# Performance work log

Hardware: AMD Instinct MI355X
Metric: run time of the kernel (lower is better)

The kernel has to match this reference:

```python
import jax, jax.numpy as jnp
import numpy as np

N, D, E = 100000, 128, 800000

def setup_inputs() -> dict:
    key = jax.random.key(0)
    k1, k2, k3, k4 = jax.random.split(key, 4)
    z = jax.random.normal(k1, (N, D), dtype=jnp.float32)
    edge_index = jax.random.randint(k2, (2, E), 0, N, dtype=jnp.int64)
    # PyTorch-style init scale for Linear layers (kaiming-uniform-ish via normal is fine for a numeric reference)
    W1 = jax.random.normal(k3, (2 * D, D), dtype=jnp.float32) * (1.0 / np.sqrt(2 * D))
    b1 = jnp.zeros((D,), dtype=jnp.float32)
    W2 = jax.random.normal(k4, (D, 1), dtype=jnp.float32) * (1.0 / np.sqrt(D))
    b2 = jnp.zeros((1,), dtype=jnp.float32)
    return {"z": z, "edge_index": edge_index, "W1": W1, "b1": b1, "W2": W2, "b2": b2}

def reference(z, edge_index, W1, b1, W2, b2):
    # row/col gather of node embeddings
    row, col = edge_index[0], edge_index[1]
    # cat([z[row], z[col]]) @ W1 == z[row] @ W1[:D] + z[col] @ W1[D:]
    # -> avoids materializing the [E, 2D] concatenated tensor
    d = z.shape[1]
    h = z[row] @ W1[:d] + z[col] @ W1[d:] + b1          # [E, D]
    h = jax.nn.relu(h)                                   # Dropout(0.1) is identity in eval mode
    out = h @ W2 + b2                                    # [E, 1]
    return out.squeeze(-1)                               # [E]
```

## Files before the change

### kernel.cpp

```cpp
#include <hip/hip_runtime.h>

#define DDIM 128

typedef __bf16 bf16x8 __attribute__((ext_vector_type(8)));
typedef float  floatx4 __attribute__((ext_vector_type(4)));

__device__ inline unsigned short f2bf(float f) {
    unsigned u = __builtin_bit_cast(unsigned, f);
    u += 0x7fffu + ((u >> 16) & 1u);
    return (unsigned short)(u >> 16);
}

#define EPI_B 136

__global__ __launch_bounds__(256) void precompute_uv_mfma_q8(
    const float* __restrict__ z, const float* __restrict__ W1,
    const float* __restrict__ b1,
    signed char* __restrict__ U8, signed char* __restrict__ V8,
    float* __restrict__ u_scale, float* __restrict__ v_scale,
    int N, int nchunks)
{
    __shared__ unsigned short WsF[32 * 64 * 8];
    __shared__ __attribute__((aligned(16))) unsigned char epi[64 * EPI_B];

    const int t    = threadIdx.x;
    const int lane = t & 63;
    const int w    = t >> 6;
    const int half = blockIdx.x;
    signed char* __restrict__ dst8 = half ? V8 : U8;
    float*       __restrict__ dscl = half ? v_scale : u_scale;
    const float* __restrict__ Wh   = W1 + (size_t)half * DDIM * DDIM;

    {
        const int nlow = lane & 15;
        const int kq   = (lane >> 4) & 3;
        #pragma unroll
        for (int i = 0; i < 8; ++i) {
            const int ntks = w + i * 4;
            const int nt = ntks >> 2, ks = ntks & 3;
            const int n  = nt * 16 + nlow;
            const int kb = ks * 32 + kq * 8;
            unsigned short frag[8];
            #pragma unroll
            for (int j = 0; j < 8; ++j)
                frag[j] = f2bf(Wh[(kb + j) * DDIM + n]);
            *(uint4*)&WsF[(ntks * 64 + lane) * 8] = *(const uint4*)frag;
        }
    }
    __syncthreads();

    const int mrow = lane & 15;
    const int quad = lane >> 4;

    float bval[8];
    #pragma unroll
    for (int nt = 0; nt < 8; ++nt)
        bval[nt] = (half == 0) ? b1[nt * 16 + mrow] : 0.f;

    for (int chunk = blockIdx.y; chunk < nchunks; chunk += gridDim.y) {
        const int m0 = chunk * 64 + w * 16;

        bf16x8 afrag[4];
        {
            int grow = m0 + mrow; if (grow > N - 1) grow = N - 1;
            const float* zrow = z + (size_t)grow * DDIM;
            #pragma unroll
            for (int ks = 0; ks < 4; ++ks) {
                const int k0 = ks * 32 + quad * 8;
                const float4 x0 = *(const float4*)(zrow + k0);
                const float4 x1 = *(const float4*)(zrow + k0 + 4);
                unsigned short a[8];
                a[0] = f2bf(x0.x); a[1] = f2bf(x0.y); a[2] = f2bf(x0.z); a[3] = f2bf(x0.w);
                a[4] = f2bf(x1.x); a[5] = f2bf(x1.y); a[6] = f2bf(x1.z); a[7] = f2bf(x1.w);
                afrag[ks] = __builtin_bit_cast(bf16x8, *(const uint4*)a);
            }
        }

        floatx4 acc[8];
        #pragma unroll
        for (int nt = 0; nt < 8; ++nt) acc[nt] = (floatx4){0.f, 0.f, 0.f, 0.f};

        #pragma unroll
        for (int ks = 0; ks < 4; ++ks) {
            #pragma unroll
            for (int nt = 0; nt < 8; ++nt) {
                const bf16x8 b = __builtin_bit_cast(bf16x8,
                    *(const uint4*)&WsF[((nt * 4 + ks) * 64 + lane) * 8]);
                acc[nt] = __builtin_amdgcn_mfma_f32_16x16x32_bf16(afrag[ks], b, acc[nt], 0, 0, 0);
            }
        }

        #pragma unroll
        for (int r = 0; r < 4; ++r) {
            float mx = 0.f;
            #pragma unroll
            for (int nt = 0; nt < 8; ++nt)
                mx = fmaxf(mx, fabsf(acc[nt][r] + bval[nt]));
            #pragma unroll
            for (int m = 1; m < 16; m <<= 1)
                mx = fmaxf(mx, __shfl_xor(mx, m, 16));
            mx = fmaxf(mx, 1e-20f);
            const float inv = 127.f / mx;

            unsigned char bytes[8];
            #pragma unroll
            for (int nt = 0; nt < 8; ++nt) {
                const float v = (acc[nt][r] + bval[nt]) * inv;
                const int q = (int)rintf(v);
                bytes[nt] = (unsigned char)(q & 0xff);
            }
            const int lrow = w * 16 + quad * 4 + r;
            *(unsigned long long*)&epi[lrow * EPI_B + mrow * 8] =
                *(const unsigned long long*)bytes;

            if (mrow == 0) {
                const int grow = chunk * 64 + lrow;
                if (grow < N) dscl[grow] = mx * (1.f / 127.f);
            }
        }
        __builtin_amdgcn_s_waitcnt(0);

        {
            const int cg = lane & 15;
            const int r2 = lane >> 4;
            #pragma unroll
            for (int it = 0; it < 4; ++it) {
                const int lr   = it * 4 + r2;
                const int lrow = w * 16 + lr;
                const uint2 dat = *(const uint2*)&epi[lrow * EPI_B + cg * 8];
                const int grow = chunk * 64 + lrow;
                if (grow < N)
                    *(uint2*)&dst8[(size_t)grow * DDIM + cg * 8] = dat;
            }
        }
    }
}

__global__ __launch_bounds__(256) void edge_kernel_i8(
    const int* __restrict__ ei,
    const signed char* __restrict__ U8, const signed char* __restrict__ V8,
    const float* __restrict__ u_scale, const float* __restrict__ v_scale,
    const float* __restrict__ W2, const float* __restrict__ b2,
    float* __restrict__ out, int E)
{
    const int t  = threadIdx.x;
    const int p  = t & 15;
    const int g0 = (blockIdx.x * 16 + (t >> 4)) * 4;

    float ww[8];
    #pragma unroll
    for (int j = 0; j < 8; ++j) ww[j] = W2[j * 16 + p];

    if (g0 >= E) return;

    int rows[4], cols[4];
    if (g0 + 3 < E) {
        const int4 r4 = *(const int4*)(ei + g0);
        const int4 c4 = *(const int4*)(ei + (size_t)E + g0);
        rows[0]=r4.x; rows[1]=r4.y; rows[2]=r4.z; rows[3]=r4.w;
        cols[0]=c4.x; cols[1]=c4.y; cols[2]=c4.z; cols[3]=c4.w;
    } else {
        #pragma unroll
        for (int i = 0; i < 4; ++i) {
            const int gi = (g0 + i < E) ? (g0 + i) : (E - 1);
            rows[i] = ei[gi];
            cols[i] = ei[(size_t)E + gi];
        }
    }

    uint2 uu[4], vv[4];
    #pragma unroll
    for (int i = 0; i < 4; ++i)
        uu[i] = *(const uint2*)(U8 + (size_t)rows[i] * DDIM + p * 8);
    #pragma unroll
    for (int i = 0; i < 4; ++i)
        vv[i] = *(const uint2*)(V8 + (size_t)cols[i] * DDIM + p * 8);

    float su[4], sv[4];
    #pragma unroll
    for (int i = 0; i < 4; ++i) { su[i] = u_scale[rows[i]]; sv[i] = v_scale[cols[i]]; }

    const float bias = b2[0];

    #pragma unroll
    for (int i = 0; i < 4; ++i) {
        const signed char* us = (const signed char*)&uu[i];
        const signed char* vs = (const signed char*)&vv[i];
        float s = 0.f;
        #pragma unroll
        for (int j = 0; j < 8; ++j) {
            const float h = fmaf(sv[i], (float)vs[j], su[i] * (float)us[j]);
            s = fmaf(fmaxf(h, 0.f), ww[j], s);
        }
        #pragma unroll
        for (int off = 8; off > 0; off >>= 1)
            s += __shfl_down(s, off, 16);
        if (p == 0 && g0 + i < E) out[g0 + i] = s + bias;
    }
}

__global__ __launch_bounds__(256) void edge_fused_fallback(
    const float* __restrict__ z, const int* __restrict__ ei,
    const float* __restrict__ W1, const float* __restrict__ b1,
    const float* __restrict__ W2, const float* __restrict__ b2,
    float* __restrict__ out, int N, int E)
{
    const int tid  = blockIdx.x * 256 + threadIdx.x;
    const int e    = tid >> 6;
    const int lane = tid & 63;
    if (e >= E) return;

    const int row = ei[e];
    const int col = ei[(size_t)E + e];
    const float* zr = z + (size_t)row * DDIM;
    const float* zc = z + (size_t)col * DDIM;

    float h0 = b1[lane];
    float h1 = b1[lane + 64];
    for (int k = 0; k < DDIM; ++k) {
        const float a = zr[k];
        const float b = zc[k];
        h0 = fmaf(a, W1[k * DDIM + lane],               h0);
        h0 = fmaf(b, W1[(DDIM + k) * DDIM + lane],      h0);
        h1 = fmaf(a, W1[k * DDIM + lane + 64],          h1);
        h1 = fmaf(b, W1[(DDIM + k) * DDIM + lane + 64], h1);
    }
    float s = fmaxf(h0, 0.f) * W2[lane] + fmaxf(h1, 0.f) * W2[lane + 64];
    #pragma unroll
    for (int off = 32; off > 0; off >>= 1)
        s += __shfl_down(s, off, 64);
    if (lane == 0) out[e] = s + b2[0];
}

extern "C" void kernel_launch(void* const* d_in, const int* in_sizes, int n_in,
                              void* d_out, int out_size, void* d_ws, size_t ws_size,
                              hipStream_t stream)
{
    const float* z  = (const float*)d_in[0];
    const int*   ei = (const int*)d_in[1];
    const float* W1 = (const float*)d_in[2];
    const float* b1 = (const float*)d_in[3];
    const float* W2 = (const float*)d_in[4];
    const float* b2 = (const float*)d_in[5];
    float*       out = (float*)d_out;

    const int N = in_sizes[0] / DDIM;
    const int E = in_sizes[1] / 2;

    const size_t n128 = (size_t)N * DDIM;
    const size_t need = 2 * n128 + 2 * (size_t)N * sizeof(float) + 256;
    if (ws_size >= need) {
        signed char* U8 = (signed char*)d_ws;
        signed char* V8 = U8 + n128;
        float* usc = (float*)(((size_t)(V8 + n128) + 255) & ~(size_t)255);
        float* vsc = usc + N;
        const int nchunks = (N + 63) / 64;
        hipLaunchKernelGGL(precompute_uv_mfma_q8, dim3(2, 384), dim3(256), 0, stream,
                           z, W1, b1, U8, V8, usc, vsc, N, nchunks);
        hipLaunchKernelGGL(edge_kernel_i8, dim3((E + 63) / 64), dim3(256), 0, stream,
                           ei, U8, V8, usc, vsc, W2, b2, out, E);
    } else {
        hipLaunchKernelGGL(edge_fused_fallback, dim3((E + 3) / 4), dim3(256), 0, stream,
                           z, ei, W1, b1, W2, b2, out, N, E);
    }
}
```

Before: 141.9 us.

## Streamline int8 quantization epilogue and bf16 conversion; switch to offset-uint8 codes

Replaces the software bf16 rounding with the packed hardware v_cvt_pk_bf16_f32 instruction. Folds the bias into the accumulator initialisation and rounds via a magic-number fma that stores offset-binary uint8 codes. Removes the LDS staging epilogue in favour of direct 8-byte global stores, uses a fast reciprocal, and changes the precompute grid size. The edge kernel decodes the unsigned bytes by subtracting a 128-based constant, which saves sign handling but relies on the magic-constant trick producing correct offset codes.

```diff
diff --git a/kernel.cpp b/kernel.cpp
--- a/kernel.cpp
+++ b/kernel.cpp
@@ -4,32 +4,23 @@
 
 typedef __bf16 bf16x8 __attribute__((ext_vector_type(8)));
 typedef float  floatx4 __attribute__((ext_vector_type(4)));
-
-__device__ inline unsigned short f2bf(float f) {
-    unsigned u = __builtin_bit_cast(unsigned, f);
-    u += 0x7fffu + ((u >> 16) & 1u);
-    return (unsigned short)(u >> 16);
-}
-
-#define EPI_B 136
 
 __global__ __launch_bounds__(256) void precompute_uv_mfma_q8(
     const float* __restrict__ z, const float* __restrict__ W1,
     const float* __restrict__ b1,
-    signed char* __restrict__ U8, signed char* __restrict__ V8,
+    unsigned char* __restrict__ U8, unsigned char* __restrict__ V8,
     float* __restrict__ u_scale, float* __restrict__ v_scale,
     int N, int nchunks)
 {
     __shared__ unsigned short WsF[32 * 64 * 8];
-    __shared__ __attribute__((aligned(16))) unsigned char epi[64 * EPI_B];
 
     const int t    = threadIdx.x;
     const int lane = t & 63;
     const int w    = t >> 6;
     const int half = blockIdx.x;
-    signed char* __restrict__ dst8 = half ? V8 : U8;
-    float*       __restrict__ dscl = half ? v_scale : u_scale;
-    const float* __restrict__ Wh   = W1 + (size_t)half * DDIM * DDIM;
+    unsigned char* __restrict__ dst8 = half ? V8 : U8;
+    float*         __restrict__ dscl = half ? v_scale : u_scale;
+    const float*   __restrict__ Wh   = W1 + (size_t)half * DDIM * DDIM;
 
     {
         const int nlow = lane & 15;
@@ -40,11 +31,16 @@
             const int nt = ntks >> 2, ks = ntks & 3;
             const int n  = nt * 16 + nlow;
             const int kb = ks * 32 + kq * 8;
-            unsigned short frag[8];
+            float f[8];
             #pragma unroll
             for (int j = 0; j < 8; ++j)
-                frag[j] = f2bf(Wh[(kb + j) * DDIM + n]);
-            *(uint4*)&WsF[(ntks * 64 + lane) * 8] = *(const uint4*)frag;
+                f[j] = Wh[(kb + j) * DDIM + n];
+            unsigned pk[4];
+            #pragma unroll
+            for (int j = 0; j < 4; ++j)
+                asm("v_cvt_pk_bf16_f32 %0, %1, %2"
+                    : "=v"(pk[j]) : "v"(f[2 * j]), "v"(f[2 * j + 1]));
+            *(uint4*)&WsF[(ntks * 64 + lane) * 8] = *(const uint4*)pk;
         }
     }
     __syncthreads();
@@ -69,16 +65,19 @@
                 const int k0 = ks * 32 + quad * 8;
                 const float4 x0 = *(const float4*)(zrow + k0);
                 const float4 x1 = *(const float4*)(zrow + k0 + 4);
-                unsigned short a[8];
-                a[0] = f2bf(x0.x); a[1] = f2bf(x0.y); a[2] = f2bf(x0.z); a[3] = f2bf(x0.w);
-                a[4] = f2bf(x1.x); a[5] = f2bf(x1.y); a[6] = f2bf(x1.z); a[7] = f2bf(x1.w);
-                afrag[ks] = __builtin_bit_cast(bf16x8, *(const uint4*)a);
+                unsigned pk[4];
+                asm("v_cvt_pk_bf16_f32 %0, %1, %2" : "=v"(pk[0]) : "v"(x0.x), "v"(x0.y));
+                asm("v_cvt_pk_bf16_f32 %0, %1, %2" : "=v"(pk[1]) : "v"(x0.z), "v"(x0.w));
+                asm("v_cvt_pk_bf16_f32 %0, %1, %2" : "=v"(pk[2]) : "v"(x1.x), "v"(x1.y));
+                asm("v_cvt_pk_bf16_f32 %0, %1, %2" : "=v"(pk[3]) : "v"(x1.z), "v"(x1.w));
+                afrag[ks] = __builtin_bit_cast(bf16x8, *(const uint4*)pk);
             }
         }
 
         floatx4 acc[8];
         #pragma unroll
-        for (int nt = 0; nt < 8; ++nt) acc[nt] = (floatx4){0.f, 0.f, 0.f, 0.f};
+        for (int nt = 0; nt < 8; ++nt)
+            acc[nt] = (floatx4){bval[nt], bval[nt], bval[nt], bval[nt]};
 
         #pragma unroll
         for (int ks = 0; ks < 4; ++ks) {
@@ -92,45 +91,28 @@
 
         #pragma unroll
         for (int r = 0; r < 4; ++r) {
-            float mx = 0.f;
-            #pragma unroll
-            for (int nt = 0; nt < 8; ++nt)
-                mx = fmaxf(mx, fabsf(acc[nt][r] + bval[nt]));
+            float mx = fmaxf(
+                fmaxf(fmaxf(fabsf(acc[0][r]), fabsf(acc[1][r])),
+                      fmaxf(fabsf(acc[2][r]), fabsf(acc[3][r]))),
+                fmaxf(fmaxf(fabsf(acc[4][r]), fabsf(acc[5][r])),
+                      fmaxf(fabsf(acc[6][r]), fabsf(acc[7][r]))));
             #pragma unroll
             for (int m = 1; m < 16; m <<= 1)
                 mx = fmaxf(mx, __shfl_xor(mx, m, 16));
             mx = fmaxf(mx, 1e-20f);
-            const float inv = 127.f / mx;
+            const float inv = 127.f * __builtin_amdgcn_rcpf(mx);
 
             unsigned char bytes[8];
             #pragma unroll
             for (int nt = 0; nt < 8; ++nt) {
-                const float v = (acc[nt][r] + bval[nt]) * inv;
-                const int q = (int)rintf(v);
-                bytes[nt] = (unsigned char)(q & 0xff);
-            }
-            const int lrow = w * 16 + quad * 4 + r;
-            *(unsigned long long*)&epi[lrow * EPI_B + mrow * 8] =
-                *(const unsigned long long*)bytes;
-
-            if (mrow == 0) {
-                const int grow = chunk * 64 + lrow;
-                if (grow < N) dscl[grow] = mx * (1.f / 127.f);
-            }
-        }
-        __builtin_amdgcn_s_waitcnt(0);
-
-        {
-            const int cg = lane & 15;
-            const int r2 = lane >> 4;
-            #pragma unroll
-            for (int it = 0; it < 4; ++it) {
-                const int lr   = it * 4 + r2;
-                const int lrow = w * 16 + lr;
-                const uint2 dat = *(const uint2*)&epi[lrow * EPI_B + cg * 8];
-                const int grow = chunk * 64 + lrow;
-                if (grow < N)
-                    *(uint2*)&dst8[(size_t)grow * DDIM + cg * 8] = dat;
+                const float fq = fmaf(acc[nt][r], inv, 12583040.0f);
+                bytes[nt] = (unsigned char)(__builtin_bit_cast(unsigned, fq) & 0xffu);
+            }
+            const int grow = chunk * 64 + w * 16 + quad * 4 + r;
+            if (grow < N) {
+                *(uint2*)&dst8[(size_t)grow * DDIM + mrow * 8] =
+                    *(const uint2*)bytes;
+                if (mrow == 0) dscl[grow] = mx * (1.f / 127.f);
             }
         }
     }
@@ -138,7 +120,7 @@
 
 __global__ __launch_bounds__(256) void edge_kernel_i8(
     const int* __restrict__ ei,
-    const signed char* __restrict__ U8, const signed char* __restrict__ V8,
+    const unsigned char* __restrict__ U8, const unsigned char* __restrict__ V8,
     const float* __restrict__ u_scale, const float* __restrict__ v_scale,
     const float* __restrict__ W2, const float* __restrict__ b2,
     float* __restrict__ out, int E)
@@ -146,12 +128,11 @@
     const int t  = threadIdx.x;
     const int p  = t & 15;
     const int g0 = (blockIdx.x * 16 + (t >> 4)) * 4;
+    if (g0 >= E) return;
 
     float ww[8];
     #pragma unroll
     for (int j = 0; j < 8; ++j) ww[j] = W2[j * 16 + p];
-
-    if (g0 >= E) return;
 
     int rows[4], cols[4];
     if (g0 + 3 < E) {
@@ -184,13 +165,23 @@
 
     #pragma unroll
     for (int i = 0; i < 4; ++i) {
-        const signed char* us = (const signed char*)&uu[i];
-        const signed char* vs = (const signed char*)&vv[i];
+        const unsigned ul = uu[i].x, uh = uu[i].y;
+        const unsigned vl = vv[i].x, vh = vv[i].y;
+        const float c = -128.f * (su[i] + sv[i]);
         float s = 0.f;
         #pragma unroll
-        for (int j = 0; j < 8; ++j) {
-            const float h = fmaf(sv[i], (float)vs[j], su[i] * (float)us[j]);
+        for (int j = 0; j < 4; ++j) {
+            const float uf = (float)((ul >> (8 * j)) & 0xffu);
+            const float vf = (float)((vl >> (8 * j)) & 0xffu);
+            const float h  = fmaf(su[i], uf, fmaf(sv[i], vf, c));
             s = fmaf(fmaxf(h, 0.f), ww[j], s);
+        }
+        #pragma unroll
+        for (int j = 0; j < 4; ++j) {
+            const float uf = (float)((uh >> (8 * j)) & 0xffu);
+            const float vf = (float)((vh >> (8 * j)) & 0xffu);
+            const float h  = fmaf(su[i], uf, fmaf(sv[i], vf, c));
+            s = fmaf(fmaxf(h, 0.f), ww[4 + j], s);
         }
         #pragma unroll
         for (int off = 8; off > 0; off >>= 1)
@@ -250,12 +241,13 @@
     const size_t n128 = (size_t)N * DDIM;
     const size_t need = 2 * n128 + 2 * (size_t)N * sizeof(float) + 256;
     if (ws_size >= need) {
-        signed char* U8 = (signed char*)d_ws;
-        signed char* V8 = U8 + n128;
+        unsigned char* U8 = (unsigned char*)d_ws;
+        unsigned char* V8 = U8 + n128;
         float* usc = (float*)(((size_t)(V8 + n128) + 255) & ~(size_t)255);
         float* vsc = usc + N;
         const int nchunks = (N + 63) / 64;
-        hipLaunchKernelGGL(precompute_uv_mfma_q8, dim3(2, 384), dim3(256), 0, stream,
+        const int gy = (nchunks + 3) / 4;
+        hipLaunchKernelGGL(precompute_uv_mfma_q8, dim3(2, gy), dim3(256), 0, stream,
                            z, W1, b1, U8, V8, usc, vsc, N, nchunks);
         hipLaunchKernelGGL(edge_kernel_i8, dim3((E + 63) / 64), dim3(256), 0, stream,
                            ei, U8, V8, usc, vsc, W2, b2, out, E);
```

After: 149.7 us. 5.5% more time.
